# Optimization experiments

Hardware: AMD Instinct MI355X
Metric: run time of the kernel (lower is better)

Reference implementation:

```python
import jax, jax.numpy as jnp
import numpy as np

B, S, D = 1, 2048, 1024
NH, NKV, HD = 16, 4, 64
N_REP = NH // NKV


def _rope_tables(seq_len, half_dim, base=10000.0):
    inv_freq = 1.0 / (base ** (np.arange(0, half_dim, dtype=np.float32) / half_dim))
    t = np.arange(seq_len, dtype=np.float32)
    freqs = np.outer(t, inv_freq)  # (S, HD//2)
    return jnp.asarray(np.cos(freqs)), jnp.asarray(np.sin(freqs))


def setup_inputs() -> dict:
    key = jax.random.key(0)
    ks = jax.random.split(key, 5)
    x = jax.random.normal(ks[0], (B, S, D), dtype=jnp.float32)
    rope_cos, rope_sin = _rope_tables(S, HD // 2)
    sd = 1.0 / np.sqrt(D)
    Wq = jax.random.normal(ks[1], (D, NH * HD), dtype=jnp.float32) * sd
    Wk = jax.random.normal(ks[2], (D, NKV * HD), dtype=jnp.float32) * sd
    Wv = jax.random.normal(ks[3], (D, NKV * HD), dtype=jnp.float32) * sd
    Wo = jax.random.normal(ks[4], (NH * HD, D), dtype=jnp.float32) * sd
    return {"x": x, "rope_cos": rope_cos, "rope_sin": rope_sin,
            "Wq": Wq, "Wk": Wk, "Wv": Wv, "Wo": Wo}


def _apply_rope(t, cos, sin):
    # t: (B, H, S, HD); cos/sin: (S, HD//2). Rotate-half convention.
    t1, t2 = jnp.split(t, 2, axis=-1)
    c = cos[None, None, :, :]
    s = sin[None, None, :, :]
    return jnp.concatenate([t1 * c - t2 * s, t2 * c + t1 * s], axis=-1)


def reference(x, rope_cos, rope_sin, Wq, Wk, Wv, Wo):
    b, s, _ = x.shape
    # projections -> (B, H, S, HD)
    q = (x @ Wq).reshape(b, s, NH, HD).transpose(0, 2, 1, 3)
    k = (x @ Wk).reshape(b, s, NKV, HD).transpose(0, 2, 1, 3)
    v = (x @ Wv).reshape(b, s, NKV, HD).transpose(0, 2, 1, 3)
    q = _apply_rope(q, rope_cos, rope_sin)
    k = _apply_rope(k, rope_cos, rope_sin)
    # GQA expansion (repeat_interleave on head axis)
    k = jnp.repeat(k, N_REP, axis=1)
    v = jnp.repeat(v, N_REP, axis=1)
    scale = HD ** -0.5
    scores = jnp.einsum('bhqd,bhkd->bhqk', q, k) * scale
    causal = jnp.tril(jnp.ones((s, s), dtype=bool))
    scores = jnp.where(causal[None, None], scores, jnp.float32(-jnp.inf))
    attn = jax.nn.softmax(scores, axis=-1)
    out = jnp.einsum('bhqk,bhkd->bhqd', attn, v)  # (B, H, S, HD)
    out = out.transpose(0, 2, 1, 3).reshape(b, s, NH * HD)
    return out @ Wo
```

## Files before the change

kernel.cpp:

```cpp
#include <hip/hip_runtime.h>

typedef unsigned short ushort_t;
typedef __attribute__((ext_vector_type(8))) short short8;
typedef __attribute__((ext_vector_type(4))) short short4v;
typedef __attribute__((ext_vector_type(4))) float f32x4;
typedef __attribute__((ext_vector_type(4))) unsigned short ushort4v;
typedef __attribute__((ext_vector_type(8))) unsigned short ushort8v;

#define S_LEN 2048
#define D_MODEL 1024
#define NH 16
#define NKV 4
#define HD 64

__device__ __forceinline__ ushort_t f2bf(float f) {
    unsigned u = __float_as_uint(f);
    u += 0x7fffu + ((u >> 16) & 1u);
    return (ushort_t)(u >> 16);
}

__device__ __forceinline__ void cp16(void* lds, const void* g) {
    __builtin_amdgcn_global_load_lds(
        (__attribute__((address_space(1))) void*)g,
        (__attribute__((address_space(3))) void*)lds, 16, 0, 0);
}

__global__ __launch_bounds__(256) void prep_kernel(
    const float* __restrict__ x, ushort_t* __restrict__ xb,
    const float* __restrict__ Wq, const float* __restrict__ Wk,
    const float* __restrict__ Wv, const float* __restrict__ Wo,
    ushort_t* __restrict__ WqT, ushort_t* __restrict__ WkT,
    ushort_t* __restrict__ WvT, ushort_t* __restrict__ WoT)
{
    const int t = threadIdx.x;
    if (blockIdx.z == 4) {
        const int b  = blockIdx.y * 16 + blockIdx.x;
        const int i0 = (b * 256 + t) * 4;
        #pragma unroll
        for (int rep = 0; rep < 8; ++rep) {
            const int i = i0 + rep * 262144;
            float4 v = *(const float4*)(x + i);
            ushort4v o = { f2bf(v.x), f2bf(v.y), f2bf(v.z), f2bf(v.w) };
            *(ushort4v*)(xb + i) = o;
        }
        return;
    }
    __shared__ ushort_t T[64 * 72];
    const float* W; ushort_t* WT; int N;
    switch (blockIdx.z) {
        case 0:  W = Wq; WT = WqT; N = 1024; break;
        case 1:  W = Wk; WT = WkT; N = 256;  break;
        case 2:  W = Wv; WT = WvT; N = 256;  break;
        default: W = Wo; WT = WoT; N = 1024; break;
    }
    const int n0 = blockIdx.y * 64;
    if (n0 >= N) return;
    const int k0 = blockIdx.x * 64;
    const int kr = t >> 4, nc = (t & 15) * 4;
    #pragma unroll
    for (int p = 0; p < 4; ++p) {
        const int k = kr + p * 16;
        float4 v = *(const float4*)(W + (size_t)(k0 + k) * N + n0 + nc);
        T[(nc + 0) * 72 + k] = f2bf(v.x);
        T[(nc + 1) * 72 + k] = f2bf(v.y);
        T[(nc + 2) * 72 + k] = f2bf(v.z);
        T[(nc + 3) * 72 + k] = f2bf(v.w);
    }
    __syncthreads();
    const int n = t >> 2, seg = (t & 3) * 16;
    ushort8v a = *(ushort8v*)&T[n * 72 + seg];
    ushort8v b = *(ushort8v*)&T[n * 72 + seg + 8];
    *(ushort8v*)(WT + (size_t)(n0 + n) * 1024 + k0 + seg)     = a;
    *(ushort8v*)(WT + (size_t)(n0 + n) * 1024 + k0 + seg + 8) = b;
}

__global__ __launch_bounds__(256, 3) void gemm_qkv_mfma(
    const ushort_t* __restrict__ xb, const ushort_t* __restrict__ WqT,
    const ushort_t* __restrict__ WkT, const ushort_t* __restrict__ WvT,
    const float* __restrict__ rc, const float* __restrict__ rs,
    ushort_t* __restrict__ Qb, ushort_t* __restrict__ Kb,
    ushort_t* __restrict__ Vtb)
{
    __shared__ ushort_t As[2][64 * 64];
    __shared__ ushort_t Bs[2][128 * 64];

    const int t = threadIdx.x;
    const int lane = t & 63, wave = t >> 6;
    const int wr = wave >> 1, wc = wave & 1;
    const int quad = lane >> 4, l15 = lane & 15;
    const int lq = lane >> 3, lr = lane & 7;
    const int swz_st = (lr ^ lq) * 8;
    const int l7 = l15 & 7;
    const int fsw0 = (quad ^ l7) * 8;
    const int fsw1 = ((quad + 4) ^ l7) * 8;

    const int m0 = blockIdx.x * 64;
    const int cy = blockIdx.y;

    const ushort_t* WT; int nloc;
    if (cy < 8)       { WT = WqT; nloc = cy * 128; }
    else if (cy < 10) { WT = WkT; nloc = (cy - 8) * 128; }
    else              { WT = WvT; nloc = (cy - 10) * 128; }

    f32x4 acc[2][4];
    #pragma unroll
    for (int i = 0; i < 2; ++i)
        #pragma unroll
        for (int j = 0; j < 4; ++j) acc[i][j] = (f32x4)0.f;

    auto stage = [&](int buf, int k0) {
        #pragma unroll
        for (int i = 0; i < 2; ++i) {
            const int r = wave * 16 + i * 8 + lq;
            cp16(&As[buf][(wave * 16 + i * 8) * 64],
                 xb + (size_t)(m0 + r) * 1024 + k0 + swz_st);
        }
        #pragma unroll
        for (int i = 0; i < 4; ++i) {
            const int r = wave * 32 + i * 8 + lq;
            cp16(&Bs[buf][(wave * 32 + i * 8) * 64],
                 WT + (size_t)(nloc + r) * 1024 + k0 + swz_st);
        }
    };

    stage(0, 0);
    __syncthreads();

    for (int kk = 0; kk < 16; ++kk) {
        const int cur = kk & 1;
        if (kk + 1 < 16) stage(cur ^ 1, (kk + 1) * 64);

        const ushort_t* Ac = &As[cur][0];
        const ushort_t* Bc = &Bs[cur][0];
        #pragma unroll
        for (int h = 0; h < 2; ++h) {
            const int fsw = h ? fsw1 : fsw0;
            short8 av[2], bv[4];
            #pragma unroll
            for (int i = 0; i < 2; ++i)
                av[i] = *(const short8*)&Ac[(wr * 32 + i * 16 + l15) * 64 + fsw];
            #pragma unroll
            for (int j = 0; j < 4; ++j)
                bv[j] = *(const short8*)&Bc[(wc * 64 + j * 16 + l15) * 64 + fsw];
            #pragma unroll
            for (int i = 0; i < 2; ++i)
                #pragma unroll
                for (int j = 0; j < 4; ++j)
                    acc[i][j] = __builtin_amdgcn_mfma_f32_16x16x32_bf16(
                        av[i], bv[j], acc[i][j], 0, 0, 0);
        }
        __syncthreads();
    }

    if (cy < 10) {
        ushort_t* dst = (cy < 8) ? Qb : Kb;
        const int h = ((cy < 8) ? cy : (cy - 8)) * 2 + wc;
        #pragma unroll
        for (int i = 0; i < 2; ++i) {
            #pragma unroll
            for (int j = 0; j < 2; ++j) {
                const int d = j * 16 + l15;
                #pragma unroll
                for (int reg = 0; reg < 4; ++reg) {
                    const int s = m0 + wr * 32 + i * 16 + quad * 4 + reg;
                    const float c  = rc[s * 32 + d];
                    const float sn = rs[s * 32 + d];
                    const float v1 = acc[i][j][reg];
                    const float v2 = acc[i][j + 2][reg];
                    dst[((size_t)h * S_LEN + s) * HD + d]      = f2bf(v1 * c - v2 * sn);
                    dst[((size_t)h * S_LEN + s) * HD + d + 32] = f2bf(v2 * c + v1 * sn);
                }
            }
        }
    } else {
        const int vh = (cy - 10) * 2 + wc;
        #pragma unroll
        for (int i = 0; i < 2; ++i) {
            const int s0 = m0 + wr * 32 + i * 16 + quad * 4;
            #pragma unroll
            for (int j = 0; j < 4; ++j) {
                const int d = j * 16 + l15;
                ushort4v o = { f2bf(acc[i][j][0]), f2bf(acc[i][j][1]),
                               f2bf(acc[i][j][2]), f2bf(acc[i][j][3]) };
                *(ushort4v*)&Vtb[((size_t)vh * HD + d) * S_LEN + s0] = o;
            }
        }
    }
}

__global__ __launch_bounds__(256, 2) void attn_mfma(
    const ushort_t* __restrict__ Qb, const ushort_t* __restrict__ Kb,
    const ushort_t* __restrict__ Vtb, ushort_t* __restrict__ attnb)
{
    __shared__ ushort_t Ks[2][2][64 * 64];
    __shared__ ushort_t Vs[2][2][64 * 64];

    const int t = threadIdx.x;
    const int lane = t & 63, wave = t >> 6;
    const int quad = lane >> 4, l15 = lane & 15;
    const int lq = lane >> 3, lr = lane & 7;
    const int swz_st = (lr ^ lq) * 8;
    const int l7 = l15 & 7;
    const int fsw0 = (quad ^ l7) * 8;
    const int fsw1 = ((quad + 4) ^ l7) * 8;

    const int vq  = quad >> 1;
    const int q14 = (quad & 1) << 2;
    const int vo0 = (((0 + vq) ^ l7) << 3) + q14;
    const int vo1 = (((2 + vq) ^ l7) << 3) + q14;
    const int vo2 = (((4 + vq) ^ l7) << 3) + q14;
    const int vo3 = (((6 + vq) ^ l7) << 3) + q14;

    const int h  = blockIdx.x;
    const int y  = blockIdx.y;
    const int qt = (y < 16) ? y : 47 - y;
    const int q0 = qt * 64;
    const int kvh = h >> 2;
    const int qrow0 = q0 + wave * 16;

    const ushort_t* Qg = Qb + ((size_t)h * S_LEN + qrow0) * HD;
    const ushort_t* Kg = Kb + (size_t)kvh * S_LEN * HD;
    const ushort_t* Vg = Vtb + (size_t)kvh * HD * S_LEN;

    short8 aq0 = *(const short8*)(Qg + (size_t)l15 * HD + quad * 8);
    short8 aq1 = *(const short8*)(Qg + (size_t)l15 * HD + 32 + quad * 8);

    float psum = 0.f;
    f32x4 Oacc[4];
    #pragma unroll
    for (int jb = 0; jb < 4; ++jb) Oacc[jb] = (f32x4)0.f;

    const int nround = (qt + 2) >> 1;

    auto stage = [&](int buf, int kvbase) {
        #pragma unroll
        for (int u = 0; u < 2; ++u)
            #pragma unroll
            for (int i = 0; i < 2; ++i) {
                const int r = wave * 16 + i * 8 + lq;
                cp16(&Ks[buf][u][(wave * 16 + i * 8) * 64],
                     Kg + (size_t)(kvbase + u * 64 + r) * 64 + swz_st);
                cp16(&Vs[buf][u][(wave * 16 + i * 8) * 64],
                     Vg + (size_t)r * 2048 + kvbase + u * 64 + swz_st);
            }
    };

    stage(0, 0);
    __syncthreads();

    for (int round = 0; round < nround; ++round) {
        const int cur = round & 1;
        if (round + 1 < nround) stage(cur ^ 1, (round + 1) * 128);

        #pragma unroll
        for (int u = 0; u < 2; ++u) {
            const int kv0 = round * 128 + u * 64;
            if (kv0 > q0 + 63) break;
            const ushort_t* Kc = &Ks[cur][u][0];
            const ushort_t* Vc = &Vs[cur][u][0];

            f32x4 sv[4];
            #pragma unroll
            for (int jb = 0; jb < 4; ++jb) {
                short8 k0 = *(const short8*)&Kc[(jb * 16 + l15) * 64 + fsw0];
                short8 k1 = *(const short8*)&Kc[(jb * 16 + l15) * 64 + fsw1];
                f32x4 z = (f32x4)0.f;
                z = __builtin_amdgcn_mfma_f32_16x16x32_bf16(k0, aq0, z, 0, 0, 0);
                z = __builtin_amdgcn_mfma_f32_16x16x32_bf16(k1, aq1, z, 0, 0, 0);
                sv[jb] = z;
            }

            const bool diag = (kv0 == q0);
            const int qg = qrow0 + l15;
            #pragma unroll
            for (int jb = 0; jb < 4; ++jb) {
                #pragma unroll
                for (int reg = 0; reg < 4; ++reg) {
                    float e = __expf(sv[jb][reg] * 0.125f);
                    if (diag && (kv0 + jb * 16 + quad * 4 + reg) > qg) e = 0.f;
                    sv[jb][reg] = e;
                    psum += e;
                }
            }

            short8 p0 = { (short)f2bf(sv[0][0]), (short)f2bf(sv[0][1]),
                          (short)f2bf(sv[0][2]), (short)f2bf(sv[0][3]),
                          (short)f2bf(sv[1][0]), (short)f2bf(sv[1][1]),
                          (short)f2bf(sv[1][2]), (short)f2bf(sv[1][3]) };
            short8 p1 = { (short)f2bf(sv[2][0]), (short)f2bf(sv[2][1]),
                          (short)f2bf(sv[2][2]), (short)f2bf(sv[2][3]),
                          (short)f2bf(sv[3][0]), (short)f2bf(sv[3][1]),
                          (short)f2bf(sv[3][2]), (short)f2bf(sv[3][3]) };

            #pragma unroll
            for (int jb = 0; jb < 4; ++jb) {
                const ushort_t* Vrow = &Vc[(jb * 16 + l15) * 64];
                short4v va0 = *(const short4v*)&Vrow[vo0];
                short4v va1 = *(const short4v*)&Vrow[vo1];
                short4v va2 = *(const short4v*)&Vrow[vo2];
                short4v va3 = *(const short4v*)&Vrow[vo3];
                short8 v0 = __builtin_shufflevector(va0, va1, 0, 1, 2, 3, 4, 5, 6, 7);
                short8 v1 = __builtin_shufflevector(va2, va3, 0, 1, 2, 3, 4, 5, 6, 7);
                Oacc[jb] = __builtin_amdgcn_mfma_f32_16x16x32_bf16(p0, v0, Oacc[jb], 0, 0, 0);
                Oacc[jb] = __builtin_amdgcn_mfma_f32_16x16x32_bf16(p1, v1, Oacc[jb], 0, 0, 0);
            }
        }

        __syncthreads();
    }

    psum += __shfl_xor(psum, 16);
    psum += __shfl_xor(psum, 32);
    #pragma unroll
    for (int reg = 0; reg < 4; ++reg) {
        const float inv = 1.f / __shfl(psum, quad * 4 + reg);
        const int s = qrow0 + quad * 4 + reg;
        #pragma unroll
        for (int jb = 0; jb < 4; ++jb)
            attnb[(size_t)s * D_MODEL + h * HD + jb * 16 + l15] =
                f2bf(Oacc[jb][reg] * inv);
    }
}

__global__ __launch_bounds__(256, 4) void gemm_out_mfma(
    const ushort_t* __restrict__ Ab, const ushort_t* __restrict__ WoT,
    float* __restrict__ out)
{
    __shared__ ushort_t As[2][64 * 64];
    __shared__ ushort_t Bs[2][64 * 64];

    const int t = threadIdx.x;
    const int lane = t & 63, wave = t >> 6;
    const int wr = wave >> 1, wc = wave & 1;
    const int quad = lane >> 4, l15 = lane & 15;
    const int lq = lane >> 3, lr = lane & 7;
    const int swz_st = (lr ^ lq) * 8;
    const int l7 = l15 & 7;
    const int fsw0 = (quad ^ l7) * 8;
    const int fsw1 = ((quad + 4) ^ l7) * 8;

    const int m0 = blockIdx.x * 64;
    const int n0 = blockIdx.y * 64;

    f32x4 acc[2][2];
    #pragma unroll
    for (int i = 0; i < 2; ++i)
        #pragma unroll
        for (int j = 0; j < 2; ++j) acc[i][j] = (f32x4)0.f;

    auto stage = [&](int buf, int k0) {
        #pragma unroll
        for (int i = 0; i < 2; ++i) {
            const int r = wave * 16 + i * 8 + lq;
            cp16(&As[buf][(wave * 16 + i * 8) * 64],
                 Ab + (size_t)(m0 + r) * 1024 + k0 + swz_st);
            cp16(&Bs[buf][(wave * 16 + i * 8) * 64],
                 WoT + (size_t)(n0 + r) * 1024 + k0 + swz_st);
        }
    };

    stage(0, 0);
    __syncthreads();

    for (int kk = 0; kk < 16; ++kk) {
        const int cur = kk & 1;
        if (kk + 1 < 16) stage(cur ^ 1, (kk + 1) * 64);

        const ushort_t* Ac = &As[cur][0];
        const ushort_t* Bc = &Bs[cur][0];
        #pragma unroll
        for (int h = 0; h < 2; ++h) {
            const int fsw = h ? fsw1 : fsw0;
            short8 av[2], bv[2];
            #pragma unroll
            for (int i = 0; i < 2; ++i)
                av[i] = *(const short8*)&Ac[(wr * 32 + i * 16 + l15) * 64 + fsw];
            #pragma unroll
            for (int j = 0; j < 2; ++j)
                bv[j] = *(const short8*)&Bc[(wc * 32 + j * 16 + l15) * 64 + fsw];
            #pragma unroll
            for (int i = 0; i < 2; ++i)
                #pragma unroll
                for (int j = 0; j < 2; ++j)
                    acc[i][j] = __builtin_amdgcn_mfma_f32_16x16x32_bf16(
                        av[i], bv[j], acc[i][j], 0, 0, 0);
        }
        __syncthreads();
    }

    #pragma unroll
    for (int i = 0; i < 2; ++i)
        #pragma unroll
        for (int reg = 0; reg < 4; ++reg) {
            const int s = m0 + wr * 32 + i * 16 + quad * 4 + reg;
            #pragma unroll
            for (int j = 0; j < 2; ++j)
                out[(size_t)s * D_MODEL + n0 + wc * 32 + j * 16 + l15] = acc[i][j][reg];
        }
}

extern "C" void kernel_launch(void* const* d_in, const int* in_sizes, int n_in,
                              void* d_out, int out_size, void* d_ws, size_t ws_size,
                              hipStream_t stream)
{
    const float* x  = (const float*)d_in[0];
    const float* rc = (const float*)d_in[1];
    const float* rs = (const float*)d_in[2];
    const float* Wq = (const float*)d_in[3];
    const float* Wk = (const float*)d_in[4];
    const float* Wv = (const float*)d_in[5];
    const float* Wo = (const float*)d_in[6];
    float* out = (float*)d_out;

    ushort_t* xb   = (ushort_t*)d_ws;
    ushort_t* WqT  = xb   + (size_t)2048 * 1024;
    ushort_t* WkT  = WqT  + (size_t)1024 * 1024;
    ushort_t* WvT  = WkT  + (size_t)256 * 1024;
    ushort_t* WoT  = WvT  + (size_t)256 * 1024;
    ushort_t* Qb   = WoT  + (size_t)1024 * 1024;
    ushort_t* Kb   = Qb   + (size_t)NH * S_LEN * HD;
    ushort_t* Vtb  = Kb   + (size_t)NKV * S_LEN * HD;
    ushort_t* attnb= Vtb  + (size_t)NKV * HD * S_LEN;

    prep_kernel<<<dim3(16, 16, 5), 256, 0, stream>>>(x, xb, Wq, Wk, Wv, Wo,
                                                     WqT, WkT, WvT, WoT);
    gemm_qkv_mfma<<<dim3(32, 12), 256, 0, stream>>>(xb, WqT, WkT, WvT,
                                                    rc, rs, Qb, Kb, Vtb);
    attn_mfma<<<dim3(NH, 32), 256, 0, stream>>>(Qb, Kb, Vtb, attnb);
    gemm_out_mfma<<<dim3(32, 16), 256, 0, stream>>>(attnb, WoT, out);
}
```

Measured before the change: 145.3 us.

## Fuse four kernels into one cooperative persistent kernel with grid syncs

Replaces the four separate launches (prep/convert, QKV GEMM with RoPE, attention, output GEMM) with a single cooperative kernel of 512 blocks that runs each stage in turn and separates them with grid.sync(). The aim is to remove launch overhead and inter-kernel gaps. In exchange, each stage is limited to a fixed 512-block grid, so the QKV stage leaves 128 blocks idle. A shared 64KB LDS buffer caps occupancy, and grid-wide barriers add their own cost.

```diff
diff --git a/kernel.cpp b/kernel.cpp
--- a/kernel.cpp
+++ b/kernel.cpp
@@ -1,4 +1,7 @@
 #include <hip/hip_runtime.h>
+#include <hip/hip_cooperative_groups.h>
+
+namespace cg = cooperative_groups;
 
 typedef unsigned short ushort_t;
 typedef __attribute__((ext_vector_type(8))) short short8;
@@ -25,176 +28,27 @@
         (__attribute__((address_space(3))) void*)lds, 16, 0, 0);
 }
 
-__global__ __launch_bounds__(256) void prep_kernel(
-    const float* __restrict__ x, ushort_t* __restrict__ xb,
+__global__ __launch_bounds__(256, 2) void fused_pipeline(
+    const float* __restrict__ x,  const float* __restrict__ rc,
+    const float* __restrict__ rs,
     const float* __restrict__ Wq, const float* __restrict__ Wk,
     const float* __restrict__ Wv, const float* __restrict__ Wo,
-    ushort_t* __restrict__ WqT, ushort_t* __restrict__ WkT,
-    ushort_t* __restrict__ WvT, ushort_t* __restrict__ WoT)
+    float* __restrict__ out, ushort_t* __restrict__ ws)
 {
-    const int t = threadIdx.x;
-    if (blockIdx.z == 4) {
-        const int b  = blockIdx.y * 16 + blockIdx.x;
-        const int i0 = (b * 256 + t) * 4;
-        #pragma unroll
-        for (int rep = 0; rep < 8; ++rep) {
-            const int i = i0 + rep * 262144;
-            float4 v = *(const float4*)(x + i);
-            ushort4v o = { f2bf(v.x), f2bf(v.y), f2bf(v.z), f2bf(v.w) };
-            *(ushort4v*)(xb + i) = o;
-        }
-        return;
-    }
-    __shared__ ushort_t T[64 * 72];
-    const float* W; ushort_t* WT; int N;
-    switch (blockIdx.z) {
-        case 0:  W = Wq; WT = WqT; N = 1024; break;
-        case 1:  W = Wk; WT = WkT; N = 256;  break;
-        case 2:  W = Wv; WT = WvT; N = 256;  break;
-        default: W = Wo; WT = WoT; N = 1024; break;
-    }
-    const int n0 = blockIdx.y * 64;
-    if (n0 >= N) return;
-    const int k0 = blockIdx.x * 64;
-    const int kr = t >> 4, nc = (t & 15) * 4;
-    #pragma unroll
-    for (int p = 0; p < 4; ++p) {
-        const int k = kr + p * 16;
-        float4 v = *(const float4*)(W + (size_t)(k0 + k) * N + n0 + nc);
-        T[(nc + 0) * 72 + k] = f2bf(v.x);
-        T[(nc + 1) * 72 + k] = f2bf(v.y);
-        T[(nc + 2) * 72 + k] = f2bf(v.z);
-        T[(nc + 3) * 72 + k] = f2bf(v.w);
-    }
-    __syncthreads();
-    const int n = t >> 2, seg = (t & 3) * 16;
-    ushort8v a = *(ushort8v*)&T[n * 72 + seg];
-    ushort8v b = *(ushort8v*)&T[n * 72 + seg + 8];
-    *(ushort8v*)(WT + (size_t)(n0 + n) * 1024 + k0 + seg)     = a;
-    *(ushort8v*)(WT + (size_t)(n0 + n) * 1024 + k0 + seg + 8) = b;
-}
-
-__global__ __launch_bounds__(256, 3) void gemm_qkv_mfma(
-    const ushort_t* __restrict__ xb, const ushort_t* __restrict__ WqT,
-    const ushort_t* __restrict__ WkT, const ushort_t* __restrict__ WvT,
-    const float* __restrict__ rc, const float* __restrict__ rs,
-    ushort_t* __restrict__ Qb, ushort_t* __restrict__ Kb,
-    ushort_t* __restrict__ Vtb)
-{
-    __shared__ ushort_t As[2][64 * 64];
-    __shared__ ushort_t Bs[2][128 * 64];
-
-    const int t = threadIdx.x;
-    const int lane = t & 63, wave = t >> 6;
-    const int wr = wave >> 1, wc = wave & 1;
-    const int quad = lane >> 4, l15 = lane & 15;
-    const int lq = lane >> 3, lr = lane & 7;
-    const int swz_st = (lr ^ lq) * 8;
-    const int l7 = l15 & 7;
-    const int fsw0 = (quad ^ l7) * 8;
-    const int fsw1 = ((quad + 4) ^ l7) * 8;
-
-    const int m0 = blockIdx.x * 64;
-    const int cy = blockIdx.y;
-
-    const ushort_t* WT; int nloc;
-    if (cy < 8)       { WT = WqT; nloc = cy * 128; }
-    else if (cy < 10) { WT = WkT; nloc = (cy - 8) * 128; }
-    else              { WT = WvT; nloc = (cy - 10) * 128; }
-
-    f32x4 acc[2][4];
-    #pragma unroll
-    for (int i = 0; i < 2; ++i)
-        #pragma unroll
-        for (int j = 0; j < 4; ++j) acc[i][j] = (f32x4)0.f;
-
-    auto stage = [&](int buf, int k0) {
-        #pragma unroll
-        for (int i = 0; i < 2; ++i) {
-            const int r = wave * 16 + i * 8 + lq;
-            cp16(&As[buf][(wave * 16 + i * 8) * 64],
-                 xb + (size_t)(m0 + r) * 1024 + k0 + swz_st);
-        }
-        #pragma unroll
-        for (int i = 0; i < 4; ++i) {
-            const int r = wave * 32 + i * 8 + lq;
-            cp16(&Bs[buf][(wave * 32 + i * 8) * 64],
-                 WT + (size_t)(nloc + r) * 1024 + k0 + swz_st);
-        }
-    };
-
-    stage(0, 0);
-    __syncthreads();
-
-    for (int kk = 0; kk < 16; ++kk) {
-        const int cur = kk & 1;
-        if (kk + 1 < 16) stage(cur ^ 1, (kk + 1) * 64);
-
-        const ushort_t* Ac = &As[cur][0];
-        const ushort_t* Bc = &Bs[cur][0];
-        #pragma unroll
-        for (int h = 0; h < 2; ++h) {
-            const int fsw = h ? fsw1 : fsw0;
-            short8 av[2], bv[4];
-            #pragma unroll
-            for (int i = 0; i < 2; ++i)
-                av[i] = *(const short8*)&Ac[(wr * 32 + i * 16 + l15) * 64 + fsw];
-            #pragma unroll
-            for (int j = 0; j < 4; ++j)
-                bv[j] = *(const short8*)&Bc[(wc * 64 + j * 16 + l15) * 64 + fsw];
-            #pragma unroll
-            for (int i = 0; i < 2; ++i)
-                #pragma unroll
-                for (int j = 0; j < 4; ++j)
-                    acc[i][j] = __builtin_amdgcn_mfma_f32_16x16x32_bf16(
-                        av[i], bv[j], acc[i][j], 0, 0, 0);
-        }
-        __syncthreads();
-    }
-
-    if (cy < 10) {
-        ushort_t* dst = (cy < 8) ? Qb : Kb;
-        const int h = ((cy < 8) ? cy : (cy - 8)) * 2 + wc;
-        #pragma unroll
-        for (int i = 0; i < 2; ++i) {
-            #pragma unroll
-            for (int j = 0; j < 2; ++j) {
-                const int d = j * 16 + l15;
-                #pragma unroll
-                for (int reg = 0; reg < 4; ++reg) {
-                    const int s = m0 + wr * 32 + i * 16 + quad * 4 + reg;
-                    const float c  = rc[s * 32 + d];
-                    const float sn = rs[s * 32 + d];
-                    const float v1 = acc[i][j][reg];
-                    const float v2 = acc[i][j + 2][reg];
-                    dst[((size_t)h * S_LEN + s) * HD + d]      = f2bf(v1 * c - v2 * sn);
-                    dst[((size_t)h * S_LEN + s) * HD + d + 32] = f2bf(v2 * c + v1 * sn);
-                }
-            }
-        }
-    } else {
-        const int vh = (cy - 10) * 2 + wc;
-        #pragma unroll
-        for (int i = 0; i < 2; ++i) {
-            const int s0 = m0 + wr * 32 + i * 16 + quad * 4;
-            #pragma unroll
-            for (int j = 0; j < 4; ++j) {
-                const int d = j * 16 + l15;
-                ushort4v o = { f2bf(acc[i][j][0]), f2bf(acc[i][j][1]),
-                               f2bf(acc[i][j][2]), f2bf(acc[i][j][3]) };
-                *(ushort4v*)&Vtb[((size_t)vh * HD + d) * S_LEN + s0] = o;
-            }
-        }
-    }
-}
-
-__global__ __launch_bounds__(256, 2) void attn_mfma(
-    const ushort_t* __restrict__ Qb, const ushort_t* __restrict__ Kb,
-    const ushort_t* __restrict__ Vtb, ushort_t* __restrict__ attnb)
-{
-    __shared__ ushort_t Ks[2][2][64 * 64];
-    __shared__ ushort_t Vs[2][2][64 * 64];
-
+    __shared__ __align__(16) char smem[65536];
+    cg::grid_group grid = cg::this_grid();
+
+    ushort_t* xb    = ws;
+    ushort_t* WqT   = xb  + (size_t)2048 * 1024;
+    ushort_t* WkT   = WqT + (size_t)1024 * 1024;
+    ushort_t* WvT   = WkT + (size_t)256 * 1024;
+    ushort_t* WoT   = WvT + (size_t)256 * 1024;
+    ushort_t* Qb    = WoT + (size_t)1024 * 1024;
+    ushort_t* Kb    = Qb  + (size_t)NH * S_LEN * HD;
+    ushort_t* Vtb   = Kb  + (size_t)NKV * S_LEN * HD;
+    ushort_t* attnb = Vtb + (size_t)NKV * HD * S_LEN;
+
+    const int bid = blockIdx.x;
     const int t = threadIdx.x;
     const int lane = t & 63, wave = t >> 6;
     const int quad = lane >> 4, l15 = lane & 15;
@@ -204,199 +58,332 @@
     const int fsw0 = (quad ^ l7) * 8;
     const int fsw1 = ((quad + 4) ^ l7) * 8;
 
-    const int vq  = quad >> 1;
-    const int q14 = (quad & 1) << 2;
-    const int vo0 = (((0 + vq) ^ l7) << 3) + q14;
-    const int vo1 = (((2 + vq) ^ l7) << 3) + q14;
-    const int vo2 = (((4 + vq) ^ l7) << 3) + q14;
-    const int vo3 = (((6 + vq) ^ l7) << 3) + q14;
-
-    const int h  = blockIdx.x;
-    const int y  = blockIdx.y;
-    const int qt = (y < 16) ? y : 47 - y;
-    const int q0 = qt * 64;
-    const int kvh = h >> 2;
-    const int qrow0 = q0 + wave * 16;
-
-    const ushort_t* Qg = Qb + ((size_t)h * S_LEN + qrow0) * HD;
-    const ushort_t* Kg = Kb + (size_t)kvh * S_LEN * HD;
-    const ushort_t* Vg = Vtb + (size_t)kvh * HD * S_LEN;
-
-    short8 aq0 = *(const short8*)(Qg + (size_t)l15 * HD + quad * 8);
-    short8 aq1 = *(const short8*)(Qg + (size_t)l15 * HD + 32 + quad * 8);
-
-    float psum = 0.f;
-    f32x4 Oacc[4];
-    #pragma unroll
-    for (int jb = 0; jb < 4; ++jb) Oacc[jb] = (f32x4)0.f;
-
-    const int nround = (qt + 2) >> 1;
-
-    auto stage = [&](int buf, int kvbase) {
+    for (int unit = bid; unit < 896; unit += 512) {
+        if (unit < 256) {
+            const int i0 = (unit * 256 + t) * 4;
+            #pragma unroll
+            for (int rep = 0; rep < 8; ++rep) {
+                const int i = i0 + rep * 262144;
+                float4 v = *(const float4*)(x + i);
+                ushort4v o = { f2bf(v.x), f2bf(v.y), f2bf(v.z), f2bf(v.w) };
+                *(ushort4v*)(xb + i) = o;
+            }
+        } else {
+            ushort_t* T = (ushort_t*)smem;
+            const int tu = unit - 256;
+            const float* W; ushort_t* WT; int N, kx, ny;
+            if (tu < 256)      { W = Wq; WT = WqT; N = 1024; kx = tu & 15;         ny = tu >> 4; }
+            else if (tu < 320) { W = Wk; WT = WkT; N = 256;  kx = (tu - 256) & 15; ny = (tu - 256) >> 4; }
+            else if (tu < 384) { W = Wv; WT = WvT; N = 256;  kx = (tu - 320) & 15; ny = (tu - 320) >> 4; }
+            else               { W = Wo; WT = WoT; N = 1024; kx = (tu - 384) & 15; ny = (tu - 384) >> 4; }
+            const int n0 = ny * 64, k0 = kx * 64;
+            const int kr = t >> 4, nc = (t & 15) * 4;
+            __syncthreads();
+            #pragma unroll
+            for (int p = 0; p < 4; ++p) {
+                const int k = kr + p * 16;
+                float4 v = *(const float4*)(W + (size_t)(k0 + k) * N + n0 + nc);
+                T[(nc + 0) * 72 + k] = f2bf(v.x);
+                T[(nc + 1) * 72 + k] = f2bf(v.y);
+                T[(nc + 2) * 72 + k] = f2bf(v.z);
+                T[(nc + 3) * 72 + k] = f2bf(v.w);
+            }
+            __syncthreads();
+            const int n = t >> 2, seg = (t & 3) * 16;
+            ushort8v a = *(ushort8v*)&T[n * 72 + seg];
+            ushort8v b = *(ushort8v*)&T[n * 72 + seg + 8];
+            *(ushort8v*)(WT + (size_t)(n0 + n) * 1024 + k0 + seg)     = a;
+            *(ushort8v*)(WT + (size_t)(n0 + n) * 1024 + k0 + seg + 8) = b;
+        }
+    }
+    grid.sync();
+
+    if (bid < 384) {
+        ushort_t* As = (ushort_t*)smem;
+        ushort_t* Bs = (ushort_t*)(smem + 16384);
+        const int wr = wave >> 1, wc = wave & 1;
+        const int m0 = (bid & 31) * 64;
+        const int cy = bid >> 5;
+
+        const ushort_t* WT; int nloc;
+        if (cy < 8)       { WT = WqT; nloc = cy * 128; }
+        else if (cy < 10) { WT = WkT; nloc = (cy - 8) * 128; }
+        else              { WT = WvT; nloc = (cy - 10) * 128; }
+
+        f32x4 acc[2][4];
         #pragma unroll
-        for (int u = 0; u < 2; ++u)
+        for (int i = 0; i < 2; ++i)
+            #pragma unroll
+            for (int j = 0; j < 4; ++j) acc[i][j] = (f32x4)0.f;
+
+        auto stage = [&](int buf, int k0) {
             #pragma unroll
             for (int i = 0; i < 2; ++i) {
                 const int r = wave * 16 + i * 8 + lq;
-                cp16(&Ks[buf][u][(wave * 16 + i * 8) * 64],
-                     Kg + (size_t)(kvbase + u * 64 + r) * 64 + swz_st);
-                cp16(&Vs[buf][u][(wave * 16 + i * 8) * 64],
-                     Vg + (size_t)r * 2048 + kvbase + u * 64 + swz_st);
-            }
-    };
-
-    stage(0, 0);
-    __syncthreads();
-
-    for (int round = 0; round < nround; ++round) {
-        const int cur = round & 1;
-        if (round + 1 < nround) stage(cur ^ 1, (round + 1) * 128);
-
+                cp16(&As[buf * 4096 + (wave * 16 + i * 8) * 64],
+                     xb + (size_t)(m0 + r) * 1024 + k0 + swz_st);
+            }
+            #pragma unroll
+            for (int i = 0; i < 4; ++i) {
+                const int r = wave * 32 + i * 8 + lq;
+                cp16(&Bs[buf * 8192 + (wave * 32 + i * 8) * 64],
+                     WT + (size_t)(nloc + r) * 1024 + k0 + swz_st);
+            }
+        };
+
+        stage(0, 0);
+        __syncthreads();
+
+        for (int kk = 0; kk < 16; ++kk) {
+            const int cur = kk & 1;
+            if (kk + 1 < 16) stage(cur ^ 1, (kk + 1) * 64);
+
+            const ushort_t* Ac = &As[cur * 4096];
+            const ushort_t* Bc = &Bs[cur * 8192];
+            #pragma unroll
+            for (int h = 0; h < 2; ++h) {
+                const int fsw = h ? fsw1 : fsw0;
+                short8 av[2], bv[4];
+                #pragma unroll
+                for (int i = 0; i < 2; ++i)
+                    av[i] = *(const short8*)&Ac[(wr * 32 + i * 16 + l15) * 64 + fsw];
+                #pragma unroll
+                for (int j = 0; j < 4; ++j)
+                    bv[j] = *(const short8*)&Bc[(wc * 64 + j * 16 + l15) * 64 + fsw];
+                #pragma unroll
+                for (int i = 0; i < 2; ++i)
+                    #pragma unroll
+                    for (int j = 0; j < 4; ++j)
+                        acc[i][j] = __builtin_amdgcn_mfma_f32_16x16x32_bf16(
+                            av[i], bv[j], acc[i][j], 0, 0, 0);
+            }
+            __syncthreads();
+        }
+
+        if (cy < 10) {
+            ushort_t* dst = (cy < 8) ? Qb : Kb;
+            const int h = ((cy < 8) ? cy : (cy - 8)) * 2 + wc;
+            #pragma unroll
+            for (int i = 0; i < 2; ++i) {
+                #pragma unroll
+                for (int j = 0; j < 2; ++j) {
+                    const int d = j * 16 + l15;
+                    #pragma unroll
+                    for (int reg = 0; reg < 4; ++reg) {
+                        const int s = m0 + wr * 32 + i * 16 + quad * 4 + reg;
+                        const float c  = rc[s * 32 + d];
+                        const float sn = rs[s * 32 + d];
+                        const float v1 = acc[i][j][reg];
+                        const float v2 = acc[i][j + 2][reg];
+                        dst[((size_t)h * S_LEN + s) * HD + d]      = f2bf(v1 * c - v2 * sn);
+                        dst[((size_t)h * S_LEN + s) * HD + d + 32] = f2bf(v2 * c + v1 * sn);
+                    }
+                }
+            }
+        } else {
+            const int vh = (cy - 10) * 2 + wc;
+            #pragma unroll
+            for (int i = 0; i < 2; ++i) {
+                const int s0 = m0 + wr * 32 + i * 16 + quad * 4;
+                #pragma unroll
+                for (int j = 0; j < 4; ++j) {
+                    const int d = j * 16 + l15;
+                    ushort4v o = { f2bf(acc[i][j][0]), f2bf(acc[i][j][1]),
+                                   f2bf(acc[i][j][2]), f2bf(acc[i][j][3]) };
+                    *(ushort4v*)&Vtb[((size_t)vh * HD + d) * S_LEN + s0] = o;
+                }
+            }
+        }
+    }
+    grid.sync();
+
+    {
+        ushort_t* Ks = (ushort_t*)smem;
+        ushort_t* Vs = (ushort_t*)(smem + 32768);
+
+        const int vq  = quad >> 1;
+        const int q14 = (quad & 1) << 2;
+        const int vo0 = (((0 + vq) ^ l7) << 3) + q14;
+        const int vo1 = (((2 + vq) ^ l7) << 3) + q14;
+        const int vo2 = (((4 + vq) ^ l7) << 3) + q14;
+        const int vo3 = (((6 + vq) ^ l7) << 3) + q14;
+
+        const int h  = bid & 15;
+        const int y  = bid >> 4;
+        const int qt = (y < 16) ? y : 47 - y;
+        const int q0 = qt * 64;
+        const int kvh = h >> 2;
+        const int qrow0 = q0 + wave * 16;
+
+        const ushort_t* Qg = Qb + ((size_t)h * S_LEN + qrow0) * HD;
+        const ushort_t* Kg = Kb + (size_t)kvh * S_LEN * HD;
+        const ushort_t* Vg = Vtb + (size_t)kvh * HD * S_LEN;
+
+        short8 aq0 = *(const short8*)(Qg + (size_t)l15 * HD + quad * 8);
+        short8 aq1 = *(const short8*)(Qg + (size_t)l15 * HD + 32 + quad * 8);
+
+        float psum = 0.f;
+        f32x4 Oacc[4];
         #pragma unroll
-        for (int u = 0; u < 2; ++u) {
-            const int kv0 = round * 128 + u * 64;
-            if (kv0 > q0 + 63) break;
-            const ushort_t* Kc = &Ks[cur][u][0];
-            const ushort_t* Vc = &Vs[cur][u][0];
-
-            f32x4 sv[4];
-            #pragma unroll
-            for (int jb = 0; jb < 4; ++jb) {
-                short8 k0 = *(const short8*)&Kc[(jb * 16 + l15) * 64 + fsw0];
-                short8 k1 = *(const short8*)&Kc[(jb * 16 + l15) * 64 + fsw1];
-                f32x4 z = (f32x4)0.f;
-                z = __builtin_amdgcn_mfma_f32_16x16x32_bf16(k0, aq0, z, 0, 0, 0);
-                z = __builtin_amdgcn_mfma_f32_16x16x32_bf16(k1, aq1, z, 0, 0, 0);
-                sv[jb] = z;
-            }
-
-            const bool diag = (kv0 == q0);
-            const int qg = qrow0 + l15;
-            #pragma unroll
-            for (int jb = 0; jb < 4; ++jb) {
-                #pragma unroll
-                for (int reg = 0; reg < 4; ++reg) {
-                    float e = __expf(sv[jb][reg] * 0.125f);
-                    if (diag && (kv0 + jb * 16 + quad * 4 + reg) > qg) e = 0.f;
-                    sv[jb][reg] = e;
-                    psum += e;
-                }
-            }
-
-            short8 p0 = { (short)f2bf(sv[0][0]), (short)f2bf(sv[0][1]),
-                          (short)f2bf(sv[0][2]), (short)f2bf(sv[0][3]),
-                          (short)f2bf(sv[1][0]), (short)f2bf(sv[1][1]),
-                          (short)f2bf(sv[1][2]), (short)f2bf(sv[1][3]) };
-            short8 p1 = { (short)f2bf(sv[2][0]), (short)f2bf(sv[2][1]),
-                          (short)f2bf(sv[2][2]), (short)f2bf(sv[2][3]),
-                          (short)f2bf(sv[3][0]), (short)f2bf(sv[3][1]),
-                          (short)f2bf(sv[3][2]), (short)f2bf(sv[3][3]) };
-
-            #pragma unroll
-            for (int jb = 0; jb < 4; ++jb) {
-                const ushort_t* Vrow = &Vc[(jb * 16 + l15) * 64];
-                short4v va0 = *(const short4v*)&Vrow[vo0];
-                short4v va1 = *(const short4v*)&Vrow[vo1];
-                short4v va2 = *(const short4v*)&Vrow[vo2];
-                short4v va3 = *(const short4v*)&Vrow[vo3];
-                short8 v0 = __builtin_shufflevector(va0, va1, 0, 1, 2, 3, 4, 5, 6, 7);
-                short8 v1 = __builtin_shufflevector(va2, va3, 0, 1, 2, 3, 4, 5, 6, 7);
-                Oacc[jb] = __builtin_amdgcn_mfma_f32_16x16x32_bf16(p0, v0, Oacc[jb], 0, 0, 0);
-                Oacc[jb] = __builtin_amdgcn_mfma_f32_16x16x32_bf16(p1, v1, Oacc[jb], 0, 0, 0);
-            }
-        }
-
+        for (int jb = 0; jb < 4; ++jb) Oacc[jb] = (f32x4)0.f;
+
+        const int nround = (qt + 2) >> 1;
+
+        auto stage = [&](int buf, int kvbase) {
+            #pragma unroll
+            for (int u = 0; u < 2; ++u)
+                #pragma unroll
+                for (int i = 0; i < 2; ++i) {
+                    const int r = wave * 16 + i * 8 + lq;
+                    cp16(&Ks[(buf * 2 + u) * 4096 + (wave * 16 + i * 8) * 64],
+                         Kg + (size_t)(kvbase + u * 64 + r) * 64 + swz_st);
+                    cp16(&Vs[(buf * 2 + u) * 4096 + (wave * 16 + i * 8) * 64],
+                         Vg + (size_t)r * 2048 + kvbase + u * 64 + swz_st);
+                }
+        };
+
+        stage(0, 0);
         __syncthreads();
-    }
-
-    psum += __shfl_xor(psum, 16);
-    psum += __shfl_xor(psum, 32);
-    #pragma unroll
-    for (int reg = 0; reg < 4; ++reg) {
-        const float inv = 1.f / __shfl(psum, quad * 4 + reg);
-        const int s = qrow0 + quad * 4 + reg;
-        #pragma unroll
-        for (int jb = 0; jb < 4; ++jb)
-            attnb[(size_t)s * D_MODEL + h * HD + jb * 16 + l15] =
-                f2bf(Oacc[jb][reg] * inv);
-    }
-}
-
-__global__ __launch_bounds__(256, 4) void gemm_out_mfma(
-    const ushort_t* __restrict__ Ab, const ushort_t* __restrict__ WoT,
-    float* __restrict__ out)
-{
-    __shared__ ushort_t As[2][64 * 64];
-    __shared__ ushort_t Bs[2][64 * 64];
-
-    const int t = threadIdx.x;
-    const int lane = t & 63, wave = t >> 6;
-    const int wr = wave >> 1, wc = wave & 1;
-    const int quad = lane >> 4, l15 = lane & 15;
-    const int lq = lane >> 3, lr = lane & 7;
-    const int swz_st = (lr ^ lq) * 8;
-    const int l7 = l15 & 7;
-    const int fsw0 = (quad ^ l7) * 8;
-    const int fsw1 = ((quad + 4) ^ l7) * 8;
-
-    const int m0 = blockIdx.x * 64;
-    const int n0 = blockIdx.y * 64;
-
-    f32x4 acc[2][2];
-    #pragma unroll
-    for (int i = 0; i < 2; ++i)
-        #pragma unroll
-        for (int j = 0; j < 2; ++j) acc[i][j] = (f32x4)0.f;
-
-    auto stage = [&](int buf, int k0) {
-        #pragma unroll
-        for (int i = 0; i < 2; ++i) {
-            const int r = wave * 16 + i * 8 + lq;
-            cp16(&As[buf][(wave * 16 + i * 8) * 64],
-                 Ab + (size_t)(m0 + r) * 1024 + k0 + swz_st);
-            cp16(&Bs[buf][(wave * 16 + i * 8) * 64],
-                 WoT + (size_t)(n0 + r) * 1024 + k0 + swz_st);
-        }
-    };
-
-    stage(0, 0);
-    __syncthreads();
-
-    for (int kk = 0; kk < 16; ++kk) {
-        const int cur = kk & 1;
-        if (kk + 1 < 16) stage(cur ^ 1, (kk + 1) * 64);
-
-        const ushort_t* Ac = &As[cur][0];
-        const ushort_t* Bc = &Bs[cur][0];
-        #pragma unroll
-        for (int h = 0; h < 2; ++h) {
-            const int fsw = h ? fsw1 : fsw0;
-            short8 av[2], bv[2];
-            #pragma unroll
-            for (int i = 0; i < 2; ++i)
-                av[i] = *(const short8*)&Ac[(wr * 32 + i * 16 + l15) * 64 + fsw];
-            #pragma unroll
-            for (int j = 0; j < 2; ++j)
-                bv[j] = *(const short8*)&Bc[(wc * 32 + j * 16 + l15) * 64 + fsw];
-            #pragma unroll
-            for (int i = 0; i < 2; ++i)
-                #pragma unroll
-                for (int j = 0; j < 2; ++j)
-                    acc[i][j] = __builtin_amdgcn_mfma_f32_16x16x32_bf16(
-                        av[i], bv[j], acc[i][j], 0, 0, 0);
-        }
-        __syncthreads();
-    }
-
-    #pragma unroll
-    for (int i = 0; i < 2; ++i)
+
+        for (int round = 0; round < nround; ++round) {
+            const int cur = round & 1;
+            if (round + 1 < nround) stage(cur ^ 1, (round + 1) * 128);
+
+            #pragma unroll
+            for (int u = 0; u < 2; ++u) {
+                const int kv0 = round * 128 + u * 64;
+                if (kv0 > q0 + 63) break;
+                const ushort_t* Kc = &Ks[(cur * 2 + u) * 4096];
+                const ushort_t* Vc = &Vs[(cur * 2 + u) * 4096];
+
+                f32x4 sv[4];
+                #pragma unroll
+                for (int jb = 0; jb < 4; ++jb) {
+                    short8 k0 = *(const short8*)&Kc[(jb * 16 + l15) * 64 + fsw0];
+                    short8 k1 = *(const short8*)&Kc[(jb * 16 + l15) * 64 + fsw1];
+                    f32x4 z = (f32x4)0.f;
+                    z = __builtin_amdgcn_mfma_f32_16x16x32_bf16(k0, aq0, z, 0, 0, 0);
+                    z = __builtin_amdgcn_mfma_f32_16x16x32_bf16(k1, aq1, z, 0, 0, 0);
+                    sv[jb] = z;
+                }
+
+                const bool diag = (kv0 == q0);
+                const int qg = qrow0 + l15;
+                #pragma unroll
+                for (int jb = 0; jb < 4; ++jb) {
+                    #pragma unroll
+                    for (int reg = 0; reg < 4; ++reg) {
+                        float e = __expf(sv[jb][reg] * 0.125f);
+                        if (diag && (kv0 + jb * 16 + quad * 4 + reg) > qg) e = 0.f;
+                        sv[jb][reg] = e;
+                        psum += e;
+                    }
+                }
+
+                short8 p0 = { (short)f2bf(sv[0][0]), (short)f2bf(sv[0][1]),
+                              (short)f2bf(sv[0][2]), (short)f2bf(sv[0][3]),
+                              (short)f2bf(sv[1][0]), (short)f2bf(sv[1][1]),
+                              (short)f2bf(sv[1][2]), (short)f2bf(sv[1][3]) };
+                short8 p1 = { (short)f2bf(sv[2][0]), (short)f2bf(sv[2][1]),
+                              (short)f2bf(sv[2][2]), (short)f2bf(sv[2][3]),
+                              (short)f2bf(sv[3][0]), (short)f2bf(sv[3][1]),
+                              (short)f2bf(sv[3][2]), (short)f2bf(sv[3][3]) };
+
+                #pragma unroll
+                for (int jb = 0; jb < 4; ++jb) {
+                    const ushort_t* Vrow = &Vc[(jb * 16 + l15) * 64];
+                    short4v va0 = *(const short4v*)&Vrow[vo0];
+                    short4v va1 = *(const short4v*)&Vrow[vo1];
+                    short4v va2 = *(const short4v*)&Vrow[vo2];
+                    short4v va3 = *(const short4v*)&Vrow[vo3];
+                    short8 v0 = __builtin_shufflevector(va0, va1, 0, 1, 2, 3, 4, 5, 6, 7);
+                    short8 v1 = __builtin_shufflevector(va2, va3, 0, 1, 2, 3, 4, 5, 6, 7);
+                    Oacc[jb] = __builtin_amdgcn_mfma_f32_16x16x32_bf16(p0, v0, Oacc[jb], 0, 0, 0);
+                    Oacc[jb] = __builtin_amdgcn_mfma_f32_16x16x32_bf16(p1, v1, Oacc[jb], 0, 0, 0);
+                }
+            }
+
+            __syncthreads();
+        }
+
+        psum += __shfl_xor(psum, 16);
+        psum += __shfl_xor(psum, 32);
         #pragma unroll
         for (int reg = 0; reg < 4; ++reg) {
-            const int s = m0 + wr * 32 + i * 16 + quad * 4 + reg;
-            #pragma unroll
-            for (int j = 0; j < 2; ++j)
-                out[(size_t)s * D_MODEL + n0 + wc * 32 + j * 16 + l15] = acc[i][j][reg];
-        }
+            const float inv = 1.f / __shfl(psum, quad * 4 + reg);
+            const int s = qrow0 + quad * 4 + reg;
+            #pragma unroll
+            for (int jb = 0; jb < 4; ++jb)
+                attnb[(size_t)s * D_MODEL + h * HD + jb * 16 + l15] =
+                    f2bf(Oacc[jb][reg] * inv);
+        }
+    }
+    grid.sync();
+
+    {
+        ushort_t* As = (ushort_t*)smem;
+        ushort_t* Bs = (ushort_t*)(smem + 16384);
+        const int wr = wave >> 1, wc = wave & 1;
+        const int m0 = (bid & 31) * 64;
+        const int n0 = (bid >> 5) * 64;
+
+        f32x4 acc[2][2];
+        #pragma unroll
+        for (int i = 0; i < 2; ++i)
+            #pragma unroll
+            for (int j = 0; j < 2; ++j) acc[i][j] = (f32x4)0.f;
+
+        auto stage = [&](int buf, int k0) {
+            #pragma unroll
+            for (int i = 0; i < 2; ++i) {
+                const int r = wave * 16 + i * 8 + lq;
+                cp16(&As[buf * 4096 + (wave * 16 + i * 8) * 64],
+                     attnb + (size_t)(m0 + r) * 1024 + k0 + swz_st);
+                cp16(&Bs[buf * 4096 + (wave * 16 + i * 8) * 64],
+                     WoT + (size_t)(n0 + r) * 1024 + k0 + swz_st);
+            }
+        };
+
+        stage(0, 0);
+        __syncthreads();
+
+        for (int kk = 0; kk < 16; ++kk) {
+            const int cur = kk & 1;
+            if (kk + 1 < 16) stage(cur ^ 1, (kk + 1) * 64);
+
+            const ushort_t* Ac = &As[cur * 4096];
+            const ushort_t* Bc = &Bs[cur * 4096];
+            #pragma unroll
+            for (int h = 0; h < 2; ++h) {
+                const int fsw = h ? fsw1 : fsw0;
+                short8 av[2], bv[2];
+                #pragma unroll
+                for (int i = 0; i < 2; ++i)
+                    av[i] = *(const short8*)&Ac[(wr * 32 + i * 16 + l15) * 64 + fsw];
+                #pragma unroll
+                for (int j = 0; j < 2; ++j)
+                    bv[j] = *(const short8*)&Bc[(wc * 32 + j * 16 + l15) * 64 + fsw];
+                #pragma unroll
+                for (int i = 0; i < 2; ++i)
+                    #pragma unroll
+                    for (int j = 0; j < 2; ++j)
+                        acc[i][j] = __builtin_amdgcn_mfma_f32_16x16x32_bf16(
+                            av[i], bv[j], acc[i][j], 0, 0, 0);
+            }
+            __syncthreads();
+        }
+
+        #pragma unroll
+        for (int i = 0; i < 2; ++i)
+            #pragma unroll
+            for (int reg = 0; reg < 4; ++reg) {
+                const int s = m0 + wr * 32 + i * 16 + quad * 4 + reg;
+                #pragma unroll
+                for (int j = 0; j < 2; ++j)
+                    out[(size_t)s * D_MODEL + n0 + wc * 32 + j * 16 + l15] =
+                        acc[i][j][reg];
+            }
+    }
 }
 
 extern "C" void kernel_launch(void* const* d_in, const int* in_sizes, int n_in,
@@ -411,21 +398,11 @@
     const float* Wv = (const float*)d_in[5];
     const float* Wo = (const float*)d_in[6];
     float* out = (float*)d_out;
-
-    ushort_t* xb   = (ushort_t*)d_ws;
-    ushort_t* WqT  = xb   + (size_t)2048 * 1024;
-    ushort_t* WkT  = WqT  + (size_t)1024 * 1024;
-    ushort_t* WvT  = WkT  + (size_t)256 * 1024;
-    ushort_t* WoT  = WvT  + (size_t)256 * 1024;
-    ushort_t* Qb   = WoT  + (size_t)1024 * 1024;
-    ushort_t* Kb   = Qb   + (size_t)NH * S_LEN * HD;
-    ushort_t* Vtb  = Kb   + (size_t)NKV * S_LEN * HD;
-    ushort_t* attnb= Vtb  + (size_t)NKV * HD * S_LEN;
-
-    prep_kernel<<<dim3(16, 16, 5), 256, 0, stream>>>(x, xb, Wq, Wk, Wv, Wo,
-                                                     WqT, WkT, WvT, WoT);
-    gemm_qkv_mfma<<<dim3(32, 12), 256, 0, stream>>>(xb, WqT, WkT, WvT,
-                                                    rc, rs, Qb, Kb, Vtb);
-    attn_mfma<<<dim3(NH, 32), 256, 0, stream>>>(Qb, Kb, Vtb, attnb);
-    gemm_out_mfma<<<dim3(32, 16), 256, 0, stream>>>(attnb, WoT, out);
+    ushort_t* ws = (ushort_t*)d_ws;
+
+    void* args[] = { (void*)&x, (void*)&rc, (void*)&rs, (void*)&Wq,
+                     (void*)&Wk, (void*)&Wv, (void*)&Wo, (void*)&out,
+                     (void*)&ws };
+    hipLaunchCooperativeKernel((void*)fused_pipeline, dim3(512), dim3(256),
+                               args, 0, stream);
 }
```

Measured after the change: 333.9 us. 130% more time.
